# Kernel tuning notes

Hardware: AMD Instinct MI355X
Metric: run time of the kernel (lower is better)

Reference implementation:

```python
import jax, jax.numpy as jnp
import numpy as np

B, N, D, NS, ITERS = 64, 4096, 256, 8, 3
EPS_ATTN = 1e-5   # module eps (added to attn)
EPS_LN = 1e-5     # torch LayerNorm default eps


def layer_norm(x, g, b):
    m = jnp.mean(x, axis=-1, keepdims=True)
    v = jnp.mean((x - m) ** 2, axis=-1, keepdims=True)
    return (x - m) / jnp.sqrt(v + EPS_LN) * g + b


def setup_inputs() -> dict:
    key = jax.random.key(0)
    ks = jax.random.split(key, 16)
    s = 0.02
    return {
        "inputs": jax.random.normal(ks[0], (B, N, D), jnp.float32),
        "slots_init": jax.random.normal(ks[1], (1, NS, D), jnp.float32),
        "Wq": jax.random.normal(ks[2], (D, D), jnp.float32) * s,
        "Wk": jax.random.normal(ks[3], (D, D), jnp.float32) * s,
        "Wv": jax.random.normal(ks[4], (D, D), jnp.float32) * s,
        "W_ih": jax.random.normal(ks[5], (3 * D, D), jnp.float32) * s,
        "W_hh": jax.random.normal(ks[6], (3 * D, D), jnp.float32) * s,
        "b_ih": jnp.zeros((3 * D,), jnp.float32),
        "b_hh": jnp.zeros((3 * D,), jnp.float32),
        "ln_in_g": jnp.ones((D,), jnp.float32),
        "ln_in_b": jnp.zeros((D,), jnp.float32),
        "ln_s_g": jnp.ones((D,), jnp.float32),
        "ln_s_b": jnp.zeros((D,), jnp.float32),
        "ln_m_g": jnp.ones((D,), jnp.float32),
        "ln_m_b": jnp.zeros((D,), jnp.float32),
        "W1": jax.random.normal(ks[7], (4 * D, D), jnp.float32) * s,
        "b1": jnp.zeros((4 * D,), jnp.float32),
        "W2": jax.random.normal(ks[8], (D, 4 * D), jnp.float32) * s,
        "b2": jnp.zeros((D,), jnp.float32),
    }


def gru_cell(x, h, W_ih, W_hh, b_ih, b_hh):
    # x, h: [M, D]; PyTorch GRU cell equations (gate order r, z, n)
    gi = x @ W_ih.T + b_ih
    gh = h @ W_hh.T + b_hh
    gi_r, gi_z, gi_n = jnp.split(gi, 3, axis=-1)
    gh_r, gh_z, gh_n = jnp.split(gh, 3, axis=-1)
    r = jax.nn.sigmoid(gi_r + gh_r)
    z = jax.nn.sigmoid(gi_z + gh_z)
    n = jnp.tanh(gi_n + r * gh_n)
    return (1.0 - z) * n + z * h


def reference(inputs, slots_init, Wq, Wk, Wv, W_ih, W_hh, b_ih, b_hh,
              ln_in_g, ln_in_b, ln_s_g, ln_s_b, ln_m_g, ln_m_b,
              W1, b1, W2, b2):
    b, n, d = inputs.shape
    scale = d ** -0.5
    slots = jnp.broadcast_to(slots_init, (b, NS, d))

    x = layer_norm(inputs, ln_in_g, ln_in_b)
    k = x @ Wk.T  # [b, n, d]
    v = x @ Wv.T  # [b, n, d]

    for _ in range(ITERS):
        slots_prev = slots
        s_n = layer_norm(slots, ln_s_g, ln_s_b)
        q = s_n @ Wq.T  # [b, ns, d]
        dots = jnp.einsum('bid,bjd->bij', q, k) * scale  # [b, ns, n]
        attn = jax.nn.softmax(dots, axis=1) + EPS_ATTN   # softmax over slots
        attn = attn / jnp.mean(attn, axis=-1, keepdims=True)
        updates = jnp.einsum('bjd,bij->bid', v, attn)     # [b, ns, d]
        h = gru_cell(updates.reshape(-1, d), slots_prev.reshape(-1, d),
                     W_ih, W_hh, b_ih, b_hh)
        slots = h.reshape(b, NS, d)
        # residual MLP with pre-norm
        y = layer_norm(slots, ln_m_g, ln_m_b)
        y = jax.nn.leaky_relu(y @ W1.T + b1, negative_slope=0.01)
        slots = slots + (y @ W2.T + b2)
    return slots
```

## Files before the change

kernel.cpp:

```cpp
#include <hip/hip_runtime.h>
#include <hip/hip_fp16.h>
#include <hip/hip_bf16.h>

#define BB 64
#define NN 4096
#define DD 256
#define NSL 8
#define NITER 3

__device__ __forceinline__ float wredsum(float v){
#pragma unroll
  for(int m=32;m;m>>=1) v += __shfl_xor(v, m, 64);
  return v;
}
__device__ __forceinline__ float2 u2f2(unsigned u){ __half2 h; __builtin_memcpy(&h,&u,4); return __half22float2(h); }
__device__ __forceinline__ float sigm(float v){ return 1.0f/(1.0f+__expf(-v)); }

union U4 { uint4 u; __half2 h[4]; };

__device__ __forceinline__ void st8(float* dst, uint4 uu){
  U4 v; v.u=uu;
  float2 f0=__half22float2(v.h[0]), f1=__half22float2(v.h[1]),
         f2=__half22float2(v.h[2]), f3=__half22float2(v.h[3]);
  dst[0]=f0.x; dst[1]=f0.y; dst[2]=f1.x; dst[3]=f1.y;
  dst[4]=f2.x; dst[5]=f2.y; dst[6]=f3.x; dst[7]=f3.y;
}

__global__ __launch_bounds__(256) void kp_all(
    const float* __restrict__ Whh, const float* __restrict__ W1,
    const float* __restrict__ W2,  const float* __restrict__ sinit,
    const float* __restrict__ Wih, const float* __restrict__ Wv,
    const float* __restrict__ Wq,  const float* __restrict__ Wk,
    __half* __restrict__ Wg, __half* __restrict__ W1t, __half* __restrict__ W2t,
    float* __restrict__ slots, __half* __restrict__ M2h, float* __restrict__ zbuf){
  int bid=blockIdx.x, t=threadIdx.x;
  if(bid<1664){
    for(int idx=bid*256+t; idx<851968; idx+=1664*256){
      if(idx<196608){ int col=idx>>8, c=idx&255; Wg[(size_t)c*1536+768+col]=__float2half(Whh[idx]); }
      else if(idx<458752){ int k=idx-196608; int col=k>>8, c=k&255; W1t[(size_t)c*1024+col]=__float2half(W1[k]); }
      else if(idx<720896){ int k=idx-458752; int col=k>>10, c=k&1023; W2t[(size_t)c*256+col]=__float2half(W2[k]); }
      else { int k=idx-720896; slots[k]=sinit[k&2047]; }
    }
  } else if(bid<2432){
    int col=bid-1664;
    __shared__ float wr[256];
    wr[t]=Wih[col*256+t];
    __syncthreads();
    float acc=0.f;
#pragma unroll 8
    for(int d=0;d<256;d++) acc += wr[d]*Wv[d*256+t];
    Wg[(size_t)t*1536+col]=__float2half(acc);
  } else if(bid<2688){
    int c=bid-2432;
    float acc=0.f;
#pragma unroll 8
    for(int d=0;d<256;d++) acc += Wq[d*256+t]*Wk[d*256+c];
    M2h[(size_t)c*256+t]=__float2half(acc*0.0625f);
  } else {
    int idx=(bid-2688)*256+t;
    if(idx<394752) zbuf[idx]=0.f;
  }
}

__global__ __launch_bounds__(256) void k_ln_x(const float* __restrict__ in, const float* __restrict__ g,
                                              const float* __restrict__ bbv, __half* __restrict__ x){
  int row  = blockIdx.x*4 + (threadIdx.x>>6);
  int lane = threadIdx.x&63;
  const float4 v = ((const float4*)(in + (size_t)row*DD))[lane];
  float s  = v.x+v.y+v.z+v.w;
  float ss = v.x*v.x+v.y*v.y+v.z*v.z+v.w*v.w;
  s = wredsum(s); ss = wredsum(ss);
  float m = s*(1.0f/256.0f);
  float r = rsqrtf(ss*(1.0f/256.0f) - m*m + 1e-5f);
  float4 gv = ((const float4*)g)[lane];
  float4 bv = ((const float4*)bbv)[lane];
  float y0=(v.x-m)*r*gv.x+bv.x, y1=(v.y-m)*r*gv.y+bv.y;
  float y2=(v.z-m)*r*gv.z+bv.z, y3=(v.w-m)*r*gv.w+bv.w;
  __half2 h0=__floats2half2_rn(y0,y1), h1=__floats2half2_rn(y2,y3);
  uint2 u; __builtin_memcpy(&u.x,&h0,4); __builtin_memcpy(&u.y,&h1,4);
  ((uint2*)(x + (size_t)row*DD))[lane] = u;
}

__global__ __launch_bounds__(256) void k_pre(const float* __restrict__ slots, const float* __restrict__ g,
                                             const float* __restrict__ bbv, const __half* __restrict__ M2h,
                                             float* __restrict__ qs, __half* __restrict__ slotsh){
  int row = blockIdx.x;
  int t = threadIdx.x;
  __shared__ __align__(16) float sn[256];
  __shared__ float red[8];
  float v = slots[row*256 + t];
  slotsh[(size_t)row*256+t]=__float2half(v);
  float s = wredsum(v), ss = wredsum(v*v);
  int wid=t>>6, lane=t&63;
  if(lane==0){ red[wid]=s; red[4+wid]=ss; }
  __syncthreads();
  float S  = red[0]+red[1]+red[2]+red[3];
  float SS = red[4]+red[5]+red[6]+red[7];
  float m = S*(1.0f/256.0f);
  float r = rsqrtf(SS*(1.0f/256.0f) - m*m + 1e-5f);
  sn[t] = (v-m)*r*g[t]+bbv[t];
  __syncthreads();
  const uint4* w4 = (const uint4*)(M2h + (size_t)t*256);
  float acc=0.f;
#pragma unroll 4
  for(int kk=0;kk<32;kk++){
    U4 w; w.u=w4[kk];
#pragma unroll
    for(int q=0;q<4;q++){
      float2 f=__half22float2(w.h[q]);
      acc += sn[kk*8+2*q]*f.x + sn[kk*8+2*q+1]*f.y;
    }
  }
  qs[row*256+t]=acc;
}

__global__ __launch_bounds__(256) void k_att(const __half* __restrict__ x, const float* __restrict__ qs,
                                             float* __restrict__ aggF, float* __restrict__ wsumF){
  int b = blockIdx.x>>4;
  int t = threadIdx.x;
  size_t j = (size_t)blockIdx.x*256 + t;
  __shared__ __align__(16) float qt[256][8];
  __shared__ __align__(16) float wl[256][8];
  __shared__ __align__(16) float aggl[4][2048];
  __shared__ float wsl[4][8];
  const float* qb = qs + b*2048;
  for(int e=t;e<2048;e+=256) qt[e&255][e>>8]=qb[e];
  __syncthreads();
  const uint4* xr = (const uint4*)(x + j*DD);
  float pd[8]={0,0,0,0,0,0,0,0};
#pragma unroll 2
  for(int ch=0; ch<32; ch++){
    uint4 u = xr[ch];
    float2 f0=u2f2(u.x), f1=u2f2(u.y), f2=u2f2(u.z), f3=u2f2(u.w);
    float xv[8]={f0.x,f0.y,f1.x,f1.y,f2.x,f2.y,f3.x,f3.y};
    int c0=ch*8;
#pragma unroll
    for(int cc=0;cc<8;cc++){
      const float4* qp=(const float4*)&qt[c0+cc][0];
      float4 qa=qp[0], qc=qp[1];
      float xvv=xv[cc];
      pd[0]+=qa.x*xvv; pd[1]+=qa.y*xvv; pd[2]+=qa.z*xvv; pd[3]+=qa.w*xvv;
      pd[4]+=qc.x*xvv; pd[5]+=qc.y*xvv; pd[6]+=qc.z*xvv; pd[7]+=qc.w*xvv;
    }
  }
  float mx=pd[0];
#pragma unroll
  for(int i=1;i<8;i++) mx=fmaxf(mx,pd[i]);
  float ev[8]; float ssum=0.f;
#pragma unroll
  for(int i=0;i<8;i++){ ev[i]=__expf(pd[i]-mx); ssum+=ev[i]; }
  float inv=1.0f/ssum;
#pragma unroll
  for(int i=0;i<8;i++) wl[t][i]=ev[i]*inv+1e-5f;
  __syncthreads();
  int wid=t>>6, lane=t&63;
  float acc[8][4];
#pragma unroll
  for(int i=0;i<8;i++){ acc[i][0]=0;acc[i][1]=0;acc[i][2]=0;acc[i][3]=0; }
  float ws[8]={0,0,0,0,0,0,0,0};
  for(int r=0;r<64;r++){
    int jl = wid*64 + r;
    uint2 u = ((const uint2*)(x + ((size_t)blockIdx.x*256 + jl)*DD))[lane];
    float2 f01=u2f2(u.x), f23=u2f2(u.y);
    const float4* wp=(const float4*)&wl[jl][0];
    float4 wa=wp[0], wb_=wp[1];
    float wv[8]={wa.x,wa.y,wa.z,wa.w,wb_.x,wb_.y,wb_.z,wb_.w};
    float xv[4]={f01.x,f01.y,f23.x,f23.y};
#pragma unroll
    for(int i=0;i<8;i++){
      acc[i][0]+=wv[i]*xv[0]; acc[i][1]+=wv[i]*xv[1];
      acc[i][2]+=wv[i]*xv[2]; acc[i][3]+=wv[i]*xv[3];
      ws[i]+=wv[i];
    }
  }
#pragma unroll
  for(int i=0;i<8;i++){
    float4 st={acc[i][0],acc[i][1],acc[i][2],acc[i][3]};
    *((float4*)&aggl[wid][i*256 + lane*4])=st;
  }
  if(lane==0){
#pragma unroll
    for(int i=0;i<8;i++) wsl[wid][i]=ws[i];
  }
  __syncthreads();
  float* ab = aggF + (size_t)b*2048;
  for(int e=t;e<2048;e+=256)
    atomicAdd(&ab[e], aggl[0][e]+aggl[1][e]+aggl[2][e]+aggl[3][e]);
  if(t<8) atomicAdd(&wsumF[b*8+t], wsl[0][t]+wsl[1][t]+wsl[2][t]+wsl[3][t]);
}

__global__ __launch_bounds__(256) void t_gates(const float* __restrict__ aggF,
    const float* __restrict__ wsumF,
    const __half* __restrict__ slotsh, const __half* __restrict__ Wg,
    const float* __restrict__ bih, const float* __restrict__ bhh,
    float* __restrict__ gl){
  int rt=blockIdx.x&15, ct=blockIdx.x>>4;
  int t=threadIdx.x;
  int r0=rt*32, c0=ct*64;
  __shared__ __align__(16) float Af[32][264];
  __shared__ __align__(16) float Wf[64][68];
  __shared__ float facS[32];
  if(ct<12){
    if(t<32) facS[t]=4096.0f/wsumF[r0+t];
    __syncthreads();
#pragma unroll
    for(int q=0;q<8;q++){
      int u=q*256+t;
      int row=u>>6, c4=u&63;
      float4 v=((const float4*)(aggF+(size_t)(r0+row)*256))[c4];
      float f=facS[row];
      v.x*=f; v.y*=f; v.z*=f; v.w*=f;
      *(float4*)&Af[row][c4*4]=v;
    }
  } else {
#pragma unroll
    for(int q=0;q<4;q++){
      int u=q*256+t;
      int row=u>>5, kk=u&31;
      st8(&Af[row][kk*8], ((const uint4*)(slotsh + ((size_t)(r0+row))*256))[kk]);
    }
  }
  float acc[2][4]={{0,0,0,0},{0,0,0,0}};
  int tx=t&15, ty=t>>4;
  for(int kc=0;kc<4;kc++){
    __syncthreads();
#pragma unroll
    for(int q=0;q<2;q++){
      int u=q*256+t;
      int kk=u>>3, cb=u&7;
      st8(&Wf[kk][cb*8], ((const uint4*)(Wg + (size_t)(kc*64+kk)*1536 + c0))[cb]);
    }
    __syncthreads();
#pragma unroll
    for(int k4=0;k4<16;k4++){
      float4 a0=*(const float4*)&Af[ty][kc*64+k4*4];
      float4 a1=*(const float4*)&Af[ty+16][kc*64+k4*4];
      float av0[4]={a0.x,a0.y,a0.z,a0.w};
      float av1[4]={a1.x,a1.y,a1.z,a1.w};
#pragma unroll
      for(int jj=0;jj<4;jj++){
        float4 wv=*(const float4*)&Wf[k4*4+jj][tx*4];
        acc[0][0]+=av0[jj]*wv.x; acc[0][1]+=av0[jj]*wv.y; acc[0][2]+=av0[jj]*wv.z; acc[0][3]+=av0[jj]*wv.w;
        acc[1][0]+=av1[jj]*wv.x; acc[1][1]+=av1[jj]*wv.y; acc[1][2]+=av1[jj]*wv.z; acc[1][3]+=av1[jj]*wv.w;
      }
    }
  }
  int col=c0+tx*4;
  const float* bb=(ct<12)? bih : bhh;
  int bcol=(ct<12)? col : col-768;
  float4 bv=*(const float4*)&bb[bcol];
  float4 o0={acc[0][0]+bv.x, acc[0][1]+bv.y, acc[0][2]+bv.z, acc[0][3]+bv.w};
  float4 o1={acc[1][0]+bv.x, acc[1][1]+bv.y, acc[1][2]+bv.z, acc[1][3]+bv.w};
  *(float4*)&gl[(size_t)(r0+ty)*1536+col]=o0;
  *(float4*)&gl[(size_t)(r0+ty+16)*1536+col]=o1;
}

__global__ __launch_bounds__(512) void t_gruln(const float* __restrict__ gl, const float* __restrict__ slots,
    const float* __restrict__ lm_g, const float* __restrict__ lm_b,
    float* __restrict__ hb, __half* __restrict__ ysh){
  int t=threadIdx.x;
  int r=t>>8, c=t&255; int row=blockIdx.x*2+r;
  __shared__ float redS[2][4], redQ[2][4];
  const float* gr = gl + (size_t)row*1536;
  float gir=gr[c], giz=gr[256+c], gin=gr[512+c];
  float ghr=gr[768+c], ghz=gr[1024+c], ghn=gr[1280+c];
  float hp = slots[(size_t)row*256+c];
  float rr=sigm(gir+ghr), z=sigm(giz+ghz);
  float n=tanhf(gin+rr*ghn);
  float hv=(1.0f-z)*n+z*hp;
  hb[(size_t)row*256+c]=hv;
  float s=wredsum(hv), ss=wredsum(hv*hv);
  if((t&63)==0){ redS[r][(t>>6)&3]=s; redQ[r][(t>>6)&3]=ss; }
  __syncthreads();
  float S=redS[r][0]+redS[r][1]+redS[r][2]+redS[r][3];
  float SS=redQ[r][0]+redQ[r][1]+redQ[r][2]+redQ[r][3];
  float m=S*(1.0f/256.0f);
  float rs=rsqrtf(SS*(1.0f/256.0f)-m*m+1e-5f);
  ysh[(size_t)row*256+c]=__float2half((hv-m)*rs*lm_g[c]+lm_b[c]);
}

__global__ __launch_bounds__(256) void t_mlp1(const __half* __restrict__ ysh,
    const __half* __restrict__ W1t, const float* __restrict__ b1,
    __half* __restrict__ z1h){
  int rt=blockIdx.x&15, ct=blockIdx.x>>4;
  int t=threadIdx.x;
  int r0=rt*32, c0=ct*64;
  __shared__ __align__(16) float Af[32][264];
  __shared__ __align__(16) float Wf[64][68];
#pragma unroll
  for(int q=0;q<4;q++){
    int u=q*256+t; int row=u>>5, kk=u&31;
    st8(&Af[row][kk*8], ((const uint4*)(ysh + ((size_t)(r0+row))*256))[kk]);
  }
  float acc[2][4]={{0,0,0,0},{0,0,0,0}};
  int tx=t&15, ty=t>>4;
  for(int kc=0;kc<4;kc++){
    __syncthreads();
#pragma unroll
    for(int q=0;q<2;q++){
      int u=q*256+t; int kk=u>>3, cb=u&7;
      st8(&Wf[kk][cb*8], ((const uint4*)(W1t + (size_t)(kc*64+kk)*1024 + c0))[cb]);
    }
    __syncthreads();
#pragma unroll
    for(int k4=0;k4<16;k4++){
      float4 a0=*(const float4*)&Af[ty][kc*64+k4*4];
      float4 a1=*(const float4*)&Af[ty+16][kc*64+k4*4];
      float av0[4]={a0.x,a0.y,a0.z,a0.w};
      float av1[4]={a1.x,a1.y,a1.z,a1.w};
#pragma unroll
      for(int jj=0;jj<4;jj++){
        float4 wv=*(const float4*)&Wf[k4*4+jj][tx*4];
        acc[0][0]+=av0[jj]*wv.x; acc[0][1]+=av0[jj]*wv.y; acc[0][2]+=av0[jj]*wv.z; acc[0][3]+=av0[jj]*wv.w;
        acc[1][0]+=av1[jj]*wv.x; acc[1][1]+=av1[jj]*wv.y; acc[1][2]+=av1[jj]*wv.z; acc[1][3]+=av1[jj]*wv.w;
      }
    }
  }
  int col=c0+tx*4;
  float4 bv=*(const float4*)&b1[col];
#pragma unroll
  for(int rr2=0;rr2<2;rr2++){
    float v0=acc[rr2][0]+bv.x, v1=acc[rr2][1]+bv.y, v2=acc[rr2][2]+bv.z, v3=acc[rr2][3]+bv.w;
    v0=v0>0.f?v0:0.01f*v0; v1=v1>0.f?v1:0.01f*v1;
    v2=v2>0.f?v2:0.01f*v2; v3=v3>0.f?v3:0.01f*v3;
    __half2 p0=__floats2half2_rn(v0,v1), p1=__floats2half2_rn(v2,v3);
    uint2 u2; __builtin_memcpy(&u2.x,&p0,4); __builtin_memcpy(&u2.y,&p1,4);
    *(uint2*)&z1h[(size_t)(r0+ty+rr2*16)*1024+col]=u2;
  }
}

__global__ __launch_bounds__(256) void t_mlp2p(const __half* __restrict__ z1h,
    const __half* __restrict__ W2t, float* __restrict__ pp){
  int b=blockIdx.x;
  int rt=b&15, ct=(b>>4)&3, kc=b>>6;
  int t=threadIdx.x;
  int r0=rt*32, c0=ct*64;
  __shared__ __align__(16) float Af[32][136];
  __shared__ __align__(16) float Wf[128][68];
#pragma unroll
  for(int q=0;q<2;q++){
    int u=q*256+t;
    int row=u>>4, seg=u&15;
    st8(&Af[row][seg*8], ((const uint4*)(z1h + (size_t)(r0+row)*1024 + kc*128))[seg]);
  }
#pragma unroll
  for(int q=0;q<4;q++){
    int u=q*256+t;
    int kk=u>>3, cb=u&7;
    st8(&Wf[kk][cb*8], ((const uint4*)(W2t + (size_t)(kc*128+kk)*256 + c0))[cb]);
  }
  __syncthreads();
  float acc[2][4]={{0,0,0,0},{0,0,0,0}};
  int tx=t&15, ty=t>>4;
#pragma unroll
  for(int k4=0;k4<32;k4++){
    float4 a0=*(const float4*)&Af[ty][k4*4];
    float4 a1=*(const float4*)&Af[ty+16][k4*4];
    float av0[4]={a0.x,a0.y,a0.z,a0.w};
    float av1[4]={a1.x,a1.y,a1.z,a1.w};
#pragma unroll
    for(int jj=0;jj<4;jj++){
      float4 wv=*(const float4*)&Wf[k4*4+jj][tx*4];
      acc[0][0]+=av0[jj]*wv.x; acc[0][1]+=av0[jj]*wv.y; acc[0][2]+=av0[jj]*wv.z; acc[0][3]+=av0[jj]*wv.w;
      acc[1][0]+=av1[jj]*wv.x; acc[1][1]+=av1[jj]*wv.y; acc[1][2]+=av1[jj]*wv.z; acc[1][3]+=av1[jj]*wv.w;
    }
  }
  int col=c0+tx*4;
  float4 o0={acc[0][0],acc[0][1],acc[0][2],acc[0][3]};
  float4 o1={acc[1][0],acc[1][1],acc[1][2],acc[1][3]};
  *(float4*)&pp[((size_t)kc*512 + r0+ty)*256+col]=o0;
  *(float4*)&pp[((size_t)kc*512 + r0+ty+16)*256+col]=o1;
}

__global__ __launch_bounds__(512) void t_fin(const float* __restrict__ hb, const float* __restrict__ pp,
    const float* __restrict__ b2, const float* __restrict__ ls_g, const float* __restrict__ ls_b,
    const __half* __restrict__ M2h, float* __restrict__ dst,
    __half* __restrict__ slotsh, float* __restrict__ qs, int last){
  int t=threadIdx.x;
  int r=t>>8, c=t&255; int row=blockIdx.x*2+r;
  __shared__ float ysl[2][256];
  __shared__ float redS[2][4], redQ[2][4];
  float s = hb[(size_t)row*256+c] + b2[c];
#pragma unroll
  for(int kc=0;kc<8;kc++) s += pp[((size_t)kc*512+row)*256+c];
  dst[(size_t)row*256+c]=s;
  if(last) return;
  slotsh[(size_t)row*256+c]=__float2half(s);
  float su=wredsum(s), sq=wredsum(s*s);
  if((t&63)==0){ redS[r][(t>>6)&3]=su; redQ[r][(t>>6)&3]=sq; }
  __syncthreads();
  float S=redS[r][0]+redS[r][1]+redS[r][2]+redS[r][3];
  float SS=redQ[r][0]+redQ[r][1]+redQ[r][2]+redQ[r][3];
  float m=S*(1.0f/256.0f);
  float rs=rsqrtf(SS*(1.0f/256.0f)-m*m+1e-5f);
  ysl[r][c]=(s-m)*rs*ls_g[c]+ls_b[c];
  __syncthreads();
  const uint4* m4=(const uint4*)(M2h+(size_t)c*256);
  float acc=0.f;
#pragma unroll 4
  for(int kk=0;kk<32;kk++){
    U4 w; w.u=m4[kk];
#pragma unroll
    for(int q=0;q<4;q++){
      float2 f=__half22float2(w.h[q]);
      acc += ysl[r][kk*8+2*q]*f.x + ysl[r][kk*8+2*q+1]*f.y;
    }
  }
  qs[(size_t)row*256+c]=acc;
}

extern "C" void kernel_launch(void* const* d_in, const int* in_sizes, int n_in,
                              void* d_out, int out_size, void* d_ws, size_t ws_size,
                              hipStream_t stream){
  const float* inputs=(const float*)d_in[0];
  const float* sinit =(const float*)d_in[1];
  const float* Wq =(const float*)d_in[2];
  const float* Wk =(const float*)d_in[3];
  const float* Wv =(const float*)d_in[4];
  const float* Wih=(const float*)d_in[5];
  const float* Whh=(const float*)d_in[6];
  const float* bih=(const float*)d_in[7];
  const float* bhh=(const float*)d_in[8];
  const float* lin_g=(const float*)d_in[9];
  const float* lin_b=(const float*)d_in[10];
  const float* ls_g=(const float*)d_in[11];
  const float* ls_b=(const float*)d_in[12];
  const float* lm_g=(const float*)d_in[13];
  const float* lm_b=(const float*)d_in[14];
  const float* W1=(const float*)d_in[15];
  const float* b1=(const float*)d_in[16];
  const float* W2=(const float*)d_in[17];
  const float* b2=(const float*)d_in[18];

  char* w=(char*)d_ws;
  __half* x    =(__half*)w; w += (size_t)BB*NN*DD*2;
  float* qs    =(float*)w;  w += 512*256*4;
  float* slots =(float*)w;  w += 512*256*4;
  __half* slotsh=(__half*)w; w += 512*256*2;
  __half* M2h  =(__half*)w; w += 256*256*2;
  __half* Wg   =(__half*)w; w += 256*1536*2;
  __half* W1t  =(__half*)w; w += 256*1024*2;
  __half* W2t  =(__half*)w; w += 1024*256*2;
  float* hb    =(float*)w;  w += 512*256*4;
  __half* ysh  =(__half*)w; w += 512*256*2;
  __half* z1h  =(__half*)w; w += (size_t)512*1024*2;
  float* pp    =(float*)w;  w += (size_t)8*512*256*4;
  float* gl_   =(float*)w;  w += (size_t)512*1536*4;
  float* aggZ  =(float*)w;  w += (size_t)(3*512*256 + 3*512)*4;

  float* aggF[3]; float* wsumF[3];
  for(int i=0;i<3;i++){ aggF[i]=aggZ + (size_t)i*512*256; wsumF[i]=aggZ + (size_t)3*512*256 + (size_t)i*512; }

  hipLaunchKernelGGL(kp_all, dim3(4230), dim3(256), 0, stream,
                     Whh, W1, W2, sinit, Wih, Wv, Wq, Wk,
                     Wg, W1t, W2t, slots, M2h, aggZ);
  hipLaunchKernelGGL(k_ln_x, dim3(65536),dim3(256), 0, stream, inputs, lin_g, lin_b, x);
  hipLaunchKernelGGL(k_pre,  dim3(512),  dim3(256), 0, stream, slots, ls_g, ls_b, M2h, qs, slotsh);
  for(int it=0; it<NITER; ++it){
    int last = (it==NITER-1);
    float* dst = last ? (float*)d_out : slots;
    hipLaunchKernelGGL(k_att,   dim3(1024), dim3(256), 0, stream, x, qs, aggF[it], wsumF[it]);
    hipLaunchKernelGGL(t_gates, dim3(384),  dim3(256), 0, stream, aggF[it], wsumF[it], slotsh, Wg, bih, bhh, gl_);
    hipLaunchKernelGGL(t_gruln, dim3(256),  dim3(512), 0, stream, gl_, slots, lm_g, lm_b, hb, ysh);
    hipLaunchKernelGGL(t_mlp1,  dim3(256),  dim3(256), 0, stream, ysh, W1t, b1, z1h);
    hipLaunchKernelGGL(t_mlp2p, dim3(512),  dim3(256), 0, stream, z1h, W2t, pp);
    hipLaunchKernelGGL(t_fin,   dim3(256),  dim3(512), 0, stream, hb, pp, b2, ls_g, ls_b, M2h,
                       dst, slotsh, qs, last);
  }
}
```

Measured before the change: 403.4 us.

## Fuse GRU+LayerNorm into MLP1 and fold final reduction into MLP2 via atomics

```diff
diff --git a/kernel.cpp b/kernel.cpp
--- a/kernel.cpp
+++ b/kernel.cpp
@@ -1,6 +1,7 @@
 #include <hip/hip_runtime.h>
 #include <hip/hip_fp16.h>
 #include <hip/hip_bf16.h>
+
 
 #define BB 64
 #define NN 4096
@@ -25,6 +26,8 @@
   dst[0]=f0.x; dst[1]=f0.y; dst[2]=f1.x; dst[3]=f1.y;
   dst[4]=f2.x; dst[5]=f2.y; dst[6]=f3.x; dst[7]=f3.y;
 }
+
+#define F8(a,b,nm) float nm[8]={a.x,a.y,a.z,a.w,b.x,b.y,b.z,b.w}
 
 __global__ __launch_bounds__(256) void kp_all(
     const float* __restrict__ Whh, const float* __restrict__ W1,
@@ -58,7 +61,7 @@
     M2h[(size_t)c*256+t]=__float2half(acc*0.0625f);
   } else {
     int idx=(bid-2688)*256+t;
-    if(idx<394752) zbuf[idx]=0.f;
+    if(idx<788160) zbuf[idx]=0.f;
   }
 }
 
@@ -255,42 +258,50 @@
   *(float4*)&gl[(size_t)(r0+ty+16)*1536+col]=o1;
 }
 
-__global__ __launch_bounds__(512) void t_gruln(const float* __restrict__ gl, const float* __restrict__ slots,
+__global__ __launch_bounds__(256) void t_mlp1g(const float* __restrict__ gl,
+    const float* __restrict__ slots,
     const float* __restrict__ lm_g, const float* __restrict__ lm_b,
-    float* __restrict__ hb, __half* __restrict__ ysh){
-  int t=threadIdx.x;
-  int r=t>>8, c=t&255; int row=blockIdx.x*2+r;
-  __shared__ float redS[2][4], redQ[2][4];
-  const float* gr = gl + (size_t)row*1536;
-  float gir=gr[c], giz=gr[256+c], gin=gr[512+c];
-  float ghr=gr[768+c], ghz=gr[1024+c], ghn=gr[1280+c];
-  float hp = slots[(size_t)row*256+c];
-  float rr=sigm(gir+ghr), z=sigm(giz+ghz);
-  float n=tanhf(gin+rr*ghn);
-  float hv=(1.0f-z)*n+z*hp;
-  hb[(size_t)row*256+c]=hv;
-  float s=wredsum(hv), ss=wredsum(hv*hv);
-  if((t&63)==0){ redS[r][(t>>6)&3]=s; redQ[r][(t>>6)&3]=ss; }
-  __syncthreads();
-  float S=redS[r][0]+redS[r][1]+redS[r][2]+redS[r][3];
-  float SS=redQ[r][0]+redQ[r][1]+redQ[r][2]+redQ[r][3];
-  float m=S*(1.0f/256.0f);
-  float rs=rsqrtf(SS*(1.0f/256.0f)-m*m+1e-5f);
-  ysh[(size_t)row*256+c]=__float2half((hv-m)*rs*lm_g[c]+lm_b[c]);
-}
-
-__global__ __launch_bounds__(256) void t_mlp1(const __half* __restrict__ ysh,
     const __half* __restrict__ W1t, const float* __restrict__ b1,
-    __half* __restrict__ z1h){
+    float* __restrict__ hb, __half* __restrict__ z1h){
   int rt=blockIdx.x&15, ct=blockIdx.x>>4;
   int t=threadIdx.x;
   int r0=rt*32, c0=ct*64;
   __shared__ __align__(16) float Af[32][264];
   __shared__ __align__(16) float Wf[64][68];
-#pragma unroll
-  for(int q=0;q<4;q++){
-    int u=q*256+t; int row=u>>5, kk=u&31;
-    st8(&Af[row][kk*8], ((const uint4*)(ysh + ((size_t)(r0+row))*256))[kk]);
+  int lane32=t&31, rowg=t>>5;
+#pragma unroll
+  for(int p=0;p<4;p++){
+    int row=p*8+rowg, gr=r0+row, c8=lane32*8;
+    const float* g=gl+(size_t)gr*1536;
+    float4 A0=*(const float4*)&g[c8],      A1=*(const float4*)&g[c8+4];      F8(A0,A1,gi);
+    float4 B0=*(const float4*)&g[256+c8],  B1=*(const float4*)&g[256+c8+4];  F8(B0,B1,gz);
+    float4 C0=*(const float4*)&g[512+c8],  C1=*(const float4*)&g[512+c8+4];  F8(C0,C1,gn);
+    float4 D0=*(const float4*)&g[768+c8],  D1=*(const float4*)&g[768+c8+4];  F8(D0,D1,hr);
+    float4 E0=*(const float4*)&g[1024+c8], E1=*(const float4*)&g[1024+c8+4]; F8(E0,E1,hz);
+    float4 G0=*(const float4*)&g[1280+c8], G1=*(const float4*)&g[1280+c8+4]; F8(G0,G1,hn);
+    float4 H0=*(const float4*)&slots[(size_t)gr*256+c8];
+    float4 H1=*(const float4*)&slots[(size_t)gr*256+c8+4]; F8(H0,H1,hp);
+    float hv8[8]; float s=0.f,qq=0.f;
+#pragma unroll
+    for(int k=0;k<8;k++){
+      float rr=sigm(gi[k]+hr[k]), zz=sigm(gz[k]+hz[k]);
+      float nn=tanhf(gn[k]+rr*hn[k]);
+      float hv=(1.0f-zz)*nn+zz*hp[k];
+      hv8[k]=hv; s+=hv; qq+=hv*hv;
+    }
+#pragma unroll
+    for(int m=16;m;m>>=1){ s+=__shfl_xor(s,m,64); qq+=__shfl_xor(qq,m,64); }
+    float mean=s*(1.0f/256.0f);
+    float rs=rsqrtf(qq*(1.0f/256.0f)-mean*mean+1e-5f);
+    float4 L0=*(const float4*)&lm_g[c8], L1=*(const float4*)&lm_g[c8+4]; F8(L0,L1,lg);
+    float4 M0=*(const float4*)&lm_b[c8], M1=*(const float4*)&lm_b[c8+4]; F8(M0,M1,lb);
+#pragma unroll
+    for(int k=0;k<8;k++) Af[row][c8+k]=(hv8[k]-mean)*rs*lg[k]+lb[k];
+    if(ct==0){
+      float4 o0={hv8[0],hv8[1],hv8[2],hv8[3]}, o1={hv8[4],hv8[5],hv8[6],hv8[7]};
+      *(float4*)&hb[(size_t)gr*256+c8]=o0;
+      *(float4*)&hb[(size_t)gr*256+c8+4]=o1;
+    }
   }
   float acc[2][4]={{0,0,0,0},{0,0,0,0}};
   int tx=t&15, ty=t>>4;
@@ -329,14 +340,20 @@
   }
 }
 
-__global__ __launch_bounds__(256) void t_mlp2p(const __half* __restrict__ z1h,
-    const __half* __restrict__ W2t, float* __restrict__ pp){
-  int b=blockIdx.x;
-  int rt=b&15, ct=(b>>4)&3, kc=b>>6;
+__global__ __launch_bounds__(256) void t_mlp2f(const __half* __restrict__ z1h,
+    const __half* __restrict__ W2t, const float* __restrict__ hb,
+    const float* __restrict__ b2, const float* __restrict__ ls_g, const float* __restrict__ ls_b,
+    const __half* __restrict__ M2h,
+    float* __restrict__ o2, int* __restrict__ cnt,
+    float* __restrict__ dst, __half* __restrict__ slotsh_w, float* __restrict__ qs, int last){
+  int bidx=blockIdx.x;
+  int rt=bidx&15, ct=(bidx>>4)&3, kc=bidx>>6;
   int t=threadIdx.x;
   int r0=rt*32, c0=ct*64;
-  __shared__ __align__(16) float Af[32][136];
-  __shared__ __align__(16) float Wf[128][68];
+  __shared__ __align__(16) char smem[52224];
+  __shared__ int lastFlag;
+  float (*Af)[136] = (float(*)[136])smem;
+  float (*Wf)[68]  = (float(*)[68])(smem + 17408);
 #pragma unroll
   for(int q=0;q<2;q++){
     int u=q*256+t;
@@ -365,48 +382,75 @@
       acc[1][0]+=av1[jj]*wv.x; acc[1][1]+=av1[jj]*wv.y; acc[1][2]+=av1[jj]*wv.z; acc[1][3]+=av1[jj]*wv.w;
     }
   }
-  int col=c0+tx*4;
-  float4 o0={acc[0][0],acc[0][1],acc[0][2],acc[0][3]};
-  float4 o1={acc[1][0],acc[1][1],acc[1][2],acc[1][3]};
-  *(float4*)&pp[((size_t)kc*512 + r0+ty)*256+col]=o0;
-  *(float4*)&pp[((size_t)kc*512 + r0+ty+16)*256+col]=o1;
-}
-
-__global__ __launch_bounds__(512) void t_fin(const float* __restrict__ hb, const float* __restrict__ pp,
-    const float* __restrict__ b2, const float* __restrict__ ls_g, const float* __restrict__ ls_b,
-    const __half* __restrict__ M2h, float* __restrict__ dst,
-    __half* __restrict__ slotsh, float* __restrict__ qs, int last){
-  int t=threadIdx.x;
-  int r=t>>8, c=t&255; int row=blockIdx.x*2+r;
-  __shared__ float ysl[2][256];
-  __shared__ float redS[2][4], redQ[2][4];
-  float s = hb[(size_t)row*256+c] + b2[c];
-#pragma unroll
-  for(int kc=0;kc<8;kc++) s += pp[((size_t)kc*512+row)*256+c];
-  dst[(size_t)row*256+c]=s;
+  {
+    int col=c0+tx*4;
+    float* p0=&o2[(size_t)(r0+ty)*256+col];
+    float* p1=&o2[(size_t)(r0+ty+16)*256+col];
+    atomicAdd(p0+0,acc[0][0]); atomicAdd(p0+1,acc[0][1]); atomicAdd(p0+2,acc[0][2]); atomicAdd(p0+3,acc[0][3]);
+    atomicAdd(p1+0,acc[1][0]); atomicAdd(p1+1,acc[1][1]); atomicAdd(p1+2,acc[1][2]); atomicAdd(p1+3,acc[1][3]);
+  }
+  __threadfence();
+  if(t==0){ int old=atomicAdd(&cnt[rt],1); lastFlag=(old==31)?1:0; }
+  __syncthreads();
+  if(!lastFlag) return;
+  __threadfence();
+  float* ysl = (float*)smem;
+  int lane32=t&31, rowg=t>>5;
+#pragma unroll
+  for(int p=0;p<4;p++){
+    int row=p*8+rowg, gr=r0+row, c8=lane32*8;
+    float4 Hh0=*(const float4*)&hb[(size_t)gr*256+c8];
+    float4 Hh1=*(const float4*)&hb[(size_t)gr*256+c8+4]; F8(Hh0,Hh1,hbv);
+    float4 O0=*(const float4*)&o2[(size_t)gr*256+c8];
+    float4 O1=*(const float4*)&o2[(size_t)gr*256+c8+4]; F8(O0,O1,ov);
+    float4 B0=*(const float4*)&b2[c8], B1=*(const float4*)&b2[c8+4]; F8(B0,B1,bv);
+    float sv8[8]; float s=0.f,qq=0.f;
+#pragma unroll
+    for(int k=0;k<8;k++){
+      float sv=hbv[k]+ov[k]+bv[k];
+      sv8[k]=sv; s+=sv; qq+=sv*sv;
+    }
+    float4 s0={sv8[0],sv8[1],sv8[2],sv8[3]}, s1={sv8[4],sv8[5],sv8[6],sv8[7]};
+    *(float4*)&dst[(size_t)gr*256+c8]=s0;
+    *(float4*)&dst[(size_t)gr*256+c8+4]=s1;
+    if(!last){
+      __half2 q0=__floats2half2_rn(sv8[0],sv8[1]), q1=__floats2half2_rn(sv8[2],sv8[3]);
+      __half2 q2=__floats2half2_rn(sv8[4],sv8[5]), q3=__floats2half2_rn(sv8[6],sv8[7]);
+      uint4 hu; __builtin_memcpy(&hu.x,&q0,4); __builtin_memcpy(&hu.y,&q1,4);
+      __builtin_memcpy(&hu.z,&q2,4); __builtin_memcpy(&hu.w,&q3,4);
+      *(uint4*)&slotsh_w[(size_t)gr*256+c8]=hu;
+#pragma unroll
+      for(int m=16;m;m>>=1){ s+=__shfl_xor(s,m,64); qq+=__shfl_xor(qq,m,64); }
+      float mean=s*(1.0f/256.0f);
+      float rs=rsqrtf(qq*(1.0f/256.0f)-mean*mean+1e-5f);
+      float4 L0=*(const float4*)&ls_g[c8], L1=*(const float4*)&ls_g[c8+4]; F8(L0,L1,lg);
+      float4 M0=*(const float4*)&ls_b[c8], M1=*(const float4*)&ls_b[c8+4]; F8(M0,M1,lb);
+#pragma unroll
+      for(int k=0;k<8;k++) ysl[row*256+c8+k]=(sv8[k]-mean)*rs*lg[k]+lb[k];
+    }
+  }
   if(last) return;
-  slotsh[(size_t)row*256+c]=__float2half(s);
-  float su=wredsum(s), sq=wredsum(s*s);
-  if((t&63)==0){ redS[r][(t>>6)&3]=su; redQ[r][(t>>6)&3]=sq; }
-  __syncthreads();
-  float S=redS[r][0]+redS[r][1]+redS[r][2]+redS[r][3];
-  float SS=redQ[r][0]+redQ[r][1]+redQ[r][2]+redQ[r][3];
-  float m=S*(1.0f/256.0f);
-  float rs=rsqrtf(SS*(1.0f/256.0f)-m*m+1e-5f);
-  ysl[r][c]=(s-m)*rs*ls_g[c]+ls_b[c];
-  __syncthreads();
-  const uint4* m4=(const uint4*)(M2h+(size_t)c*256);
-  float acc=0.f;
-#pragma unroll 4
-  for(int kk=0;kk<32;kk++){
-    U4 w; w.u=m4[kk];
-#pragma unroll
-    for(int q=0;q<4;q++){
-      float2 f=__half22float2(w.h[q]);
-      acc += ysl[r][kk*8+2*q]*f.x + ysl[r][kk*8+2*q+1]*f.y;
-    }
-  }
-  qs[(size_t)row*256+c]=acc;
+  __syncthreads();
+  {
+    float acc2[32];
+#pragma unroll
+    for(int r=0;r<32;r++) acc2[r]=0.f;
+    const uint4* m4=(const uint4*)(M2h+(size_t)t*256);
+    for(int kk=0;kk<32;kk++){
+      U4 w; w.u=m4[kk];
+      float2 f0=__half22float2(w.h[0]), f1=__half22float2(w.h[1]);
+      float2 f2=__half22float2(w.h[2]), f3=__half22float2(w.h[3]);
+      float w8[8]={f0.x,f0.y,f1.x,f1.y,f2.x,f2.y,f3.x,f3.y};
+#pragma unroll
+      for(int r=0;r<32;r++){
+        const float* yr=&ysl[r*256+kk*8];
+        acc2[r]+=w8[0]*yr[0]+w8[1]*yr[1]+w8[2]*yr[2]+w8[3]*yr[3]
+                +w8[4]*yr[4]+w8[5]*yr[5]+w8[6]*yr[6]+w8[7]*yr[7];
+      }
+    }
+#pragma unroll
+    for(int r=0;r<32;r++) qs[(size_t)(r0+r)*256+t]=acc2[r];
+  }
 }
 
 extern "C" void kernel_launch(void* const* d_in, const int* in_sizes, int n_in,
@@ -442,16 +486,19 @@
   __half* W1t  =(__half*)w; w += 256*1024*2;
   __half* W2t  =(__half*)w; w += 1024*256*2;
   float* hb    =(float*)w;  w += 512*256*4;
-  __half* ysh  =(__half*)w; w += 512*256*2;
   __half* z1h  =(__half*)w; w += (size_t)512*1024*2;
-  float* pp    =(float*)w;  w += (size_t)8*512*256*4;
   float* gl_   =(float*)w;  w += (size_t)512*1536*4;
-  float* aggZ  =(float*)w;  w += (size_t)(3*512*256 + 3*512)*4;
-
-  float* aggF[3]; float* wsumF[3];
-  for(int i=0;i<3;i++){ aggF[i]=aggZ + (size_t)i*512*256; wsumF[i]=aggZ + (size_t)3*512*256 + (size_t)i*512; }
-
-  hipLaunchKernelGGL(kp_all, dim3(4230), dim3(256), 0, stream,
+  float* aggZ  =(float*)w;  w += (size_t)788160*4;
+
+  float* aggFv[3]; float* wsumFv[3]; float* o2v[3]; int* cntv[3];
+  for(int i=0;i<3;i++){
+    aggFv[i]  = aggZ + (size_t)i*131072;
+    wsumFv[i] = aggZ + 393216 + (size_t)i*512;
+    o2v[i]    = aggZ + 394752 + (size_t)i*131072;
+    cntv[i]   = (int*)(aggZ + 787968 + (size_t)i*64);
+  }
+
+  hipLaunchKernelGGL(kp_all, dim3(5767), dim3(256), 0, stream,
                      Whh, W1, W2, sinit, Wih, Wv, Wq, Wk,
                      Wg, W1t, W2t, slots, M2h, aggZ);
   hipLaunchKernelGGL(k_ln_x, dim3(65536),dim3(256), 0, stream, inputs, lin_g, lin_b, x);
@@ -459,12 +506,10 @@
   for(int it=0; it<NITER; ++it){
     int last = (it==NITER-1);
     float* dst = last ? (float*)d_out : slots;
-    hipLaunchKernelGGL(k_att,   dim3(1024), dim3(256), 0, stream, x, qs, aggF[it], wsumF[it]);
-    hipLaunchKernelGGL(t_gates, dim3(384),  dim3(256), 0, stream, aggF[it], wsumF[it], slotsh, Wg, bih, bhh, gl_);
-    hipLaunchKernelGGL(t_gruln, dim3(256),  dim3(512), 0, stream, gl_, slots, lm_g, lm_b, hb, ysh);
-    hipLaunchKernelGGL(t_mlp1,  dim3(256),  dim3(256), 0, stream, ysh, W1t, b1, z1h);
-    hipLaunchKernelGGL(t_mlp2p, dim3(512),  dim3(256), 0, stream, z1h, W2t, pp);
-    hipLaunchKernelGGL(t_fin,   dim3(256),  dim3(512), 0, stream, hb, pp, b2, ls_g, ls_b, M2h,
-                       dst, slotsh, qs, last);
-  }
-}
+    hipLaunchKernelGGL(k_att,   dim3(1024), dim3(256), 0, stream, x, qs, aggFv[it], wsumFv[it]);
+    hipLaunchKernelGGL(t_gates, dim3(384),  dim3(256), 0, stream, aggFv[it], wsumFv[it], slotsh, Wg, bih, bhh, gl_);
+    hipLaunchKernelGGL(t_mlp1g, dim3(256),  dim3(256), 0, stream, gl_, slots, lm_g, lm_b, W1t, b1, hb, z1h);
+    hipLaunchKernelGGL(t_mlp2f, dim3(512),  dim3(256), 0, stream, z1h, W2t, hb, b2, ls_g, ls_b, M2h,
+                       o2v[it], cntv[it], dst, slotsh, qs, last);
+  }
+}
```

Measured after the change: 582.7 us. +44.4%, slower.
